# Kernel optimization log

Measured on AMD Instinct MI355X. Metric: run time of the kernel, lower is better.

## Reference

```python
import jax, jax.numpy as jnp
import numpy as np

EPS = 1e-5


def conv2d(x, w, b=None, stride=1, padding=0, dilation=1, groups=1):
    out = jax.lax.conv_general_dilated(
        x, w, (stride, stride), [(padding, padding), (padding, padding)],
        rhs_dilation=(dilation, dilation),
        dimension_numbers=('NCHW', 'OIHW', 'NCHW'),
        feature_group_count=groups)
    if b is not None:
        out = out + b[None, :, None, None]
    return out


def unfold3(x):
    # torch nn.Unfold(kernel=3, padding=1), kept as [b, c, 9, h, w]
    # (channel-major ordering c*9+k, k = row-major kernel index, matches torch)
    b, c, h, w = x.shape
    xp = jnp.pad(x, ((0, 0), (0, 0), (1, 1), (1, 1)))
    return jnp.stack([xp[:, :, i:i + h, j:j + w]
                      for i in range(3) for j in range(3)], axis=2)


def setup_inputs():
    B, C, O, H, W = 8, 64, 64, 128, 128
    key = jax.random.key(0)
    ks = jax.random.split(key, 16)
    s = 0.05
    rn = lambda k, shape: jax.random.normal(k, shape, jnp.float32) * s
    return {
        'x': jax.random.normal(ks[0], (B, C, H, W), jnp.float32),
        'cdcm_conv1_w': rn(ks[1], (C, C, 1, 1)),
        'cdcm_conv1_b': jnp.zeros((C,), jnp.float32),
        'cdcm_w5': rn(ks[2], (C, C, 3, 3)),
        'cdcm_w7': rn(ks[3], (C, C, 3, 3)),
        'cdcm_w9': rn(ks[4], (C, C, 3, 3)),
        'cdcm_w11': rn(ks[5], (C, C, 3, 3)),
        'dsc_dw_w': rn(ks[6], (C, 1, 3, 3)),
        'dsc_dw_b': jnp.zeros((C,), jnp.float32),
        'dsc_pw_w': rn(ks[7], (C, C, 1, 1)),
        'dsc_pw_b': jnp.zeros((C,), jnp.float32),
        'gw_w': rn(ks[8], (C, 9, 9)),
        'gw_b': jnp.zeros((C, 9), jnp.float32),
        'gw_bn_g': jnp.ones((C, 9), jnp.float32),
        'gw_bn_b': jnp.zeros((C, 9), jnp.float32),
        'gw_bn_m': jnp.zeros((C, 9), jnp.float32),
        'gw_bn_v': jnp.ones((C, 9), jnp.float32),
        'conv_w': rn(ks[9], (O, C, 3, 3)),
        'conv_b': jnp.zeros((O,), jnp.float32),
        'fr_w': rn(ks[10], (O, O, 1, 1)),
        'fr_b': jnp.zeros((O,), jnp.float32),
        'ens_w': rn(ks[11], (3, O, O, 3, 3)),
        'ens_b': jnp.zeros((3, O), jnp.float32),
        'bn_g': jnp.ones((O,), jnp.float32),
        'bn_b': jnp.zeros((O,), jnp.float32),
        'bn_m': jnp.zeros((O,), jnp.float32),
        'bn_v': jnp.ones((O,), jnp.float32),
    }


def reference(x, cdcm_conv1_w, cdcm_conv1_b, cdcm_w5, cdcm_w7, cdcm_w9, cdcm_w11,
              dsc_dw_w, dsc_dw_b, dsc_pw_w, dsc_pw_b,
              gw_w, gw_b, gw_bn_g, gw_bn_b, gw_bn_m, gw_bn_v,
              conv_w, conv_b, fr_w, fr_b, ens_w, ens_b,
              bn_g, bn_b, bn_m, bn_v):
    C = x.shape[1]
    # ---- CDCM: relu -> 1x1 conv -> 4 dilated 3x3 convs, each through the
    # SAME DepthwiseSeparableConv instance, then summed ----
    y = conv2d(jax.nn.relu(x), cdcm_conv1_w, cdcm_conv1_b)

    def dsc(z):
        z = conv2d(z, dsc_dw_w, dsc_dw_b, padding=1, groups=C)
        return conv2d(z, dsc_pw_w, dsc_pw_b)

    y = sum(dsc(conv2d(y, w, padding=d, dilation=d))
            for w, d in ((cdcm_w5, 5), (cdcm_w7, 7), (cdcm_w9, 9), (cdcm_w11, 11)))

    b, c, h, w = y.shape
    patches = unfold3(y)  # [b, c, 9, h, w]

    # ---- dynamic weight generation: grouped 1x1 conv (groups=c, 9->9 per
    # group) + inference BatchNorm over the c*9 channels + softmax over the 9
    # patch positions ----
    gw = jnp.einsum('coi,bcihw->bcohw', gw_w, patches) + gw_b[None, :, :, None, None]
    scale = (gw_bn_g / jnp.sqrt(gw_bn_v + EPS))[None, :, :, None, None]
    gw = (gw - gw_bn_m[None, :, :, None, None]) * scale + gw_bn_b[None, :, :, None, None]
    wsm = jax.nn.softmax(gw, axis=2)

    # ---- involution core: the rearrange to (3h,3w) + stride-3 3x3 conv is
    # exactly a contraction of (patches * weights) with the conv kernel over
    # the 9 kernel positions (row-major kernel index == patch index) ----
    prod = patches * wsm  # [b, c, 9, h, w]
    O = conv_w.shape[0]
    out = jnp.einsum('bckhw,ock->bohw', prod, conv_w.reshape(O, c, 9)) + conv_b[None, :, None, None]

    # ---- feature reuse: conv1x1(conv_out) + conv_out ----
    out = conv2d(out, fr_w, fr_b) + out

    # ---- ensemble: mean of 3 conv3x3 ----
    out = jnp.mean(jnp.stack([conv2d(out, ens_w[i], ens_b[i], padding=1)
                              for i in range(3)]), axis=0)

    # ---- final BN (inference) + ReLU ----
    out = (out - bn_m[None, :, None, None]) * (bn_g / jnp.sqrt(bn_v + EPS))[None, :, None, None] \
          + bn_b[None, :, None, None]
    return jax.nn.relu(out)
```

## Files before the change

### kernel.cpp

```cpp
#include <hip/hip_runtime.h>
#include <hip/hip_bf16.h>
#include <hip/hip_fp16.h>

#define EPSV 1e-5f
#define Bn 8
#define Cn 64
#define Hn 128
#define Wn 128
#define Pn (Hn*Wn)
#define PR 150
#define PE 130
#define YPAD_ELEMS (Bn*PR*PR*Cn)

typedef _Float16 v8h __attribute__((ext_vector_type(8)));
typedef float v16f __attribute__((ext_vector_type(16)));
typedef unsigned short ushort8v __attribute__((ext_vector_type(8)));
typedef unsigned short ushort4v __attribute__((ext_vector_type(4)));

__device__ __forceinline__ unsigned short f2h(float v) {
  _Float16 h = (_Float16)v;
  return *reinterpret_cast<const unsigned short*>(&h);
}
__device__ __forceinline__ float h2f(unsigned short u) {
  return (float)(*reinterpret_cast<const _Float16*>(&u));
}

__device__ __forceinline__ v8h exp8h(v8h x) {
  union { v8h v; __half2 h[4]; } u; u.v = x;
  #pragma unroll
  for (int i = 0; i < 4; i++) u.h[i] = h2exp(u.h[i]);
  return u.v;
}
__device__ __forceinline__ v8h rcp8h(v8h x) {
  union { v8h v; __half2 h[4]; } u; u.v = x;
  #pragma unroll
  for (int i = 0; i < 4; i++) u.h[i] = h2rcp(u.h[i]);
  return u.v;
}

__device__ __forceinline__ size_t clb(int b, int row, int kb, int col, int PD) {
  return ((((size_t)b * PD + row) * 4 + kb) * PD + col) * 16;
}

__device__ __forceinline__ void swz_bh(int& b, int& h) {
  int bid = blockIdx.x;
  int w = (bid & 7) * 128 + (bid >> 3);
  b = w >> 7; h = w & 127;
}

__global__ __launch_bounds__(256) void k_prep(
    const float* __restrict__ w1, const float* __restrict__ w5,
    const float* __restrict__ w7, const float* __restrict__ w9,
    const float* __restrict__ w11, const float* __restrict__ pww,
    const float* __restrict__ frw, const float* __restrict__ cw,
    const float* __restrict__ gww, const float* __restrict__ gwb,
    const float* __restrict__ gbg, const float* __restrict__ gbb,
    const float* __restrict__ gbm, const float* __restrict__ gbv,
    const float* __restrict__ ensw, const float* __restrict__ ensb,
    const float* __restrict__ bng, const float* __restrict__ bnb,
    const float* __restrict__ bnm, const float* __restrict__ bnv,
    unsigned short* __restrict__ apack, unsigned short* __restrict__ apinv,
    unsigned short* __restrict__ apens, unsigned short* __restrict__ appw1,
    unsigned short* __restrict__ appw, unsigned short* __restrict__ apfr,
    unsigned short* __restrict__ gwpk,
    unsigned short* __restrict__ apk, unsigned short* __restrict__ bpk,
    float* __restrict__ esc, float* __restrict__ ebi)
{
  int id = blockIdx.x * 256 + threadIdx.x;
  if (id < 147456) {
    int e = id & 7, l = (id >> 3) & 63, mh = (id >> 9) & 1,
        kb = (id >> 10) & 3, tap = id >> 12;
    int d = tap / 9, k9 = tap - 9 * d;
    int m = mh * 32 + (l & 31);
    int c = kb * 16 + (l >> 5) * 8 + e;
    const float* src = (d == 0) ? w5 : (d == 1) ? w7 : (d == 2) ? w9 : w11;
    apack[id] = f2h(src[(m * 64 + c) * 9 + k9]);
    return;
  }
  id -= 147456;
  if (id < 36864) {
    int e = id & 7, l = (id >> 3) & 63, mh = (id >> 9) & 1,
        kb = (id >> 10) & 3, tap = id >> 12;
    int m = mh * 32 + (l & 31);
    int c = kb * 16 + (l >> 5) * 8 + e;
    apinv[id] = f2h(cw[(m * 64 + c) * 9 + tap]);
    return;
  }
  id -= 36864;
  if (id < 36864) {
    int e = id & 7, l = (id >> 3) & 63, mh = (id >> 9) & 1,
        kb = (id >> 10) & 3, tap = id >> 12;
    int m = mh * 32 + (l & 31);
    int c = kb * 16 + (l >> 5) * 8 + e;
    float v = (ensw[((0 * 64 + m) * 64 + c) * 9 + tap] +
               ensw[((64 + m) * 64 + c) * 9 + tap] +
               ensw[((128 + m) * 64 + c) * 9 + tap]) * (1.f / 3.f);
    apens[id] = f2h(v);
    return;
  }
  id -= 36864;
  if (id < 4096) {
    int e = id & 7, l = (id >> 3) & 63, mh = (id >> 9) & 1, kb = (id >> 10) & 3;
    int m = mh * 32 + (l & 31);
    int c = kb * 16 + (l >> 5) * 8 + e;
    appw1[id] = f2h(w1[m * 64 + c]);
    return;
  }
  id -= 4096;
  if (id < 4096) {
    int e = id & 7, l = (id >> 3) & 63, mh = (id >> 9) & 1, kb = (id >> 10) & 3;
    int m = mh * 32 + (l & 31);
    int c = kb * 16 + (l >> 5) * 8 + e;
    appw[id] = f2h(pww[m * 64 + c]);
    return;
  }
  id -= 4096;
  if (id < 4096) {
    int e = id & 7, l = (id >> 3) & 63, mh = (id >> 9) & 1, kb = (id >> 10) & 3;
    int m = mh * 32 + (l & 31);
    int c = kb * 16 + (l >> 5) * 8 + e;
    apfr[id] = f2h(frw[m * 64 + c]);
    return;
  }
  id -= 4096;
  if (id < 5184) {
    int cblk = id / 648, r = id - cblk * 648;
    int tap = r >> 3, ch = r & 7;
    int c = cblk * 8 + ch;
    gwpk[id] = f2h(gww[c * 81 + tap]);
    return;
  }
  id -= 5184;
  if (id < 576) {
    int cblk = id / 72, r = id - cblk * 72;
    int o = r >> 3, ch = r & 7;
    int c = cblk * 8 + ch;
    float A = gbg[c * 9 + o] / sqrtf(gbv[c * 9 + o] + EPSV);
    apk[id] = f2h(A);
    return;
  }
  id -= 576;
  if (id < 576) {
    int cblk = id / 72, r = id - cblk * 72;
    int o = r >> 3, ch = r & 7;
    int c = cblk * 8 + ch;
    float A = gbg[c * 9 + o] / sqrtf(gbv[c * 9 + o] + EPSV);
    float B = (gwb[c * 9 + o] - gbm[c * 9 + o]) * A + gbb[c * 9 + o];
    bpk[id] = f2h(B);
    return;
  }
  id -= 576;
  if (id < 64) {
    float s = bng[id] / sqrtf(bnv[id] + EPSV);
    esc[id] = s;
    float bm = (ensb[id] + ensb[64 + id] + ensb[128 + id]) * (1.f / 3.f);
    ebi[id] = (bm - bnm[id]) * s + bnb[id];
  }
}

__global__ __launch_bounds__(256) void k_zb(unsigned short* __restrict__ buf,
                                            int PD, int pad)
{
  int per_b = 2 * pad * PD + 128 * 2 * pad;
  int id = blockIdx.x * 256 + threadIdx.x;
  int b = id / per_b;
  if (b >= Bn) return;
  int r = id - b * per_b;
  int tb = 2 * pad * PD;
  int row, col;
  if (r < tb) {
    int rr = r / PD; col = r - rr * PD;
    row = (rr < pad) ? rr : (rr + 128);
  } else {
    int r2 = r - tb;
    row = pad + r2 / (2 * pad);
    int cc = r2 - (r2 / (2 * pad)) * (2 * pad);
    col = (cc < pad) ? cc : (cc + 128);
  }
  ushort8v z = {0, 0, 0, 0, 0, 0, 0, 0};
  #pragma unroll
  for (int kb = 0; kb < 4; kb++) {
    unsigned short* p = buf + clb(b, row, kb, col, PD);
    *(ushort8v*)p = z;
    *(ushort8v*)(p + 8) = z;
  }
}

__global__ __launch_bounds__(256, 4) void k_pw1x(const float* __restrict__ x,
    const unsigned short* __restrict__ apw, const float* __restrict__ bias,
    unsigned short* __restrict__ ypad)
{
  int b, h; swz_bh(b, h);
  const int tid = threadIdx.x, wv = tid >> 6, l = tid & 63;
  const int ln31 = l & 31, g = l >> 5;
  const int px = wv * 32 + ln31;
  const float* xb = x + ((size_t)b * Cn) * Pn + h * Wn + px;
  v16f acc0, acc1;
  #pragma unroll
  for (int r = 0; r < 16; r++) { acc0[r] = 0.f; acc1[r] = 0.f; }
  const unsigned short* apl = apw + l * 8;
  #pragma unroll
  for (int kb = 0; kb < 4; kb++) {
    int c0 = kb * 16 + g * 8;
    v8h Bf;
    #pragma unroll
    for (int e = 0; e < 8; e++)
      Bf[e] = (_Float16)fmaxf(xb[(size_t)(c0 + e) * Pn], 0.f);
    v8h A0 = *(const v8h*)(apl + (kb * 2) * 512);
    v8h A1 = *(const v8h*)(apl + (kb * 2 + 1) * 512);
    acc0 = __builtin_amdgcn_mfma_f32_32x32x16_f16(A0, Bf, acc0, 0, 0, 0);
    acc1 = __builtin_amdgcn_mfma_f32_32x32x16_f16(A1, Bf, acc1, 0, 0, 0);
  }
  #pragma unroll
  for (int t = 0; t < 4; t++) {
    int c0 = 8 * t + 4 * g;
    int kb = c0 >> 4, sub = c0 & 15;
    ushort4v s0, s1;
    #pragma unroll
    for (int u = 0; u < 4; u++) {
      s0[u] = f2h(acc0[4 * t + u] + bias[c0 + u]);
      s1[u] = f2h(acc1[4 * t + u] + bias[c0 + u + 32]);
    }
    *(ushort4v*)(ypad + clb(b, h + 11, kb, px + 11, PR) + sub) = s0;
    *(ushort4v*)(ypad + clb(b, h + 11, kb + 2, px + 11, PR) + sub) = s1;
  }
}

__global__ __launch_bounds__(256) void k_cdcm_mfma(
    const unsigned short* __restrict__ ypad,
    const unsigned short* __restrict__ apack,
    unsigned short* __restrict__ spad)
{
  __shared__ __align__(16) unsigned short Abuf[36864];
  const int bid = blockIdx.x;
  const int b = bid & 7, h0 = (bid >> 3) * 2;
  const int tid = threadIdx.x, wv = tid >> 6, l = tid & 63;
  const int ln31 = l & 31, g = l >> 5;

  v16f a00, a01, a10, a11;
  #pragma unroll
  for (int r = 0; r < 16; r++) { a00[r] = 0.f; a01[r] = 0.f; a10[r] = 0.f; a11[r] = 0.f; }

  const unsigned short* abl = Abuf + l * 8;

  for (int d = 0; d < 4; d++) {
    __syncthreads();
    {
      const ushort8v* src = (const ushort8v*)(apack + d * 36864);
      ushort8v* dst = (ushort8v*)Abuf;
      #pragma unroll
      for (int it = 0; it < 18; it++)
        dst[tid + it * 256] = src[tid + it * 256];
    }
    __syncthreads();

    const int dil = 5 + 2 * d;
    #pragma unroll
    for (int ky = 0; ky < 3; ky++) {
      const int r0 = h0 + 11 + (ky - 1) * dil;
      #pragma unroll
      for (int kx = 0; kx < 3; kx++) {
        const int col = wv * 32 + ln31 + (kx - 1) * dil + 11;
        const int t9 = ky * 3 + kx;
        const unsigned short* ap = abl + t9 * 4096;
        #pragma unroll
        for (int kb = 0; kb < 4; kb++) {
          v8h B0 = *(const v8h*)(ypad + clb(b, r0, kb, col, PR) + g * 8);
          v8h B1 = *(const v8h*)(ypad + clb(b, r0 + 1, kb, col, PR) + g * 8);
          v8h A0 = *(const v8h*)(ap + kb * 1024);
          v8h A1 = *(const v8h*)(ap + kb * 1024 + 512);
          a00 = __builtin_amdgcn_mfma_f32_32x32x16_f16(A0, B0, a00, 0, 0, 0);
          a01 = __builtin_amdgcn_mfma_f32_32x32x16_f16(A1, B0, a01, 0, 0, 0);
          a10 = __builtin_amdgcn_mfma_f32_32x32x16_f16(A0, B1, a10, 0, 0, 0);
          a11 = __builtin_amdgcn_mfma_f32_32x32x16_f16(A1, B1, a11, 0, 0, 0);
        }
      }
    }
  }
  const int px = wv * 32 + ln31;
  #pragma unroll
  for (int t = 0; t < 4; t++) {
    int c0 = 8 * t + 4 * g;
    int kb = c0 >> 4, sub = c0 & 15;
    ushort4v s0, s1, s2, s3;
    #pragma unroll
    for (int u = 0; u < 4; u++) {
      s0[u] = f2h(a00[4 * t + u]);
      s1[u] = f2h(a01[4 * t + u]);
      s2[u] = f2h(a10[4 * t + u]);
      s3[u] = f2h(a11[4 * t + u]);
    }
    *(ushort4v*)(spad + clb(b, h0 + 1, kb, px + 1, PE) + sub) = s0;
    *(ushort4v*)(spad + clb(b, h0 + 1, kb + 2, px + 1, PE) + sub) = s1;
    *(ushort4v*)(spad + clb(b, h0 + 2, kb, px + 1, PE) + sub) = s2;
    *(ushort4v*)(spad + clb(b, h0 + 2, kb + 2, px + 1, PE) + sub) = s3;
  }
}

__global__ __launch_bounds__(256, 4) void k_dwpw_mfma(
    const unsigned short* __restrict__ spad,
    const float* __restrict__ dww, const float* __restrict__ dwb,
    const unsigned short* __restrict__ appw, const float* __restrict__ pwb,
    unsigned short* __restrict__ y2pad)
{
  __shared__ float wdw[576];
  __shared__ float bdw[64];
  const int tid = threadIdx.x;
  for (int t = tid; t < 576; t += 256) wdw[t] = dww[t];
  if (tid < 64) bdw[tid] = dwb[tid];
  __syncthreads();

  int b, h; swz_bh(b, h);
  const int wv = tid >> 6, l = tid & 63;
  const int ln31 = l & 31, g = l >> 5;
  const int w = wv * 32 + ln31;

  v16f acc0, acc1;
  #pragma unroll
  for (int r = 0; r < 16; r++) { acc0[r] = 0.f; acc1[r] = 0.f; }
  const unsigned short* apl = appw + l * 8;

  #pragma unroll
  for (int kb = 0; kb < 4; kb++) {
    const int c0 = kb * 16 + g * 8;
    v8h t[9];
    #pragma unroll
    for (int k = 0; k < 9; k++) {
      const int dy = k / 3 - 1, dx = k % 3 - 1;
      t[k] = *(const v8h*)(spad + clb(b, h + 1 + dy, kb, w + 1 + dx, PE) + g * 8);
    }
    v8h dvh;
    #pragma unroll
    for (int e = 0; e < 8; e++) {
      const int c = c0 + e;
      float a = 4.f * bdw[c];
      #pragma unroll
      for (int k = 0; k < 9; k++) a += wdw[c * 9 + k] * (float)t[k][e];
      dvh[e] = (_Float16)a;
    }
    v8h A0 = *(const v8h*)(apl + (kb * 2) * 512);
    v8h A1 = *(const v8h*)(apl + (kb * 2 + 1) * 512);
    acc0 = __builtin_amdgcn_mfma_f32_32x32x16_f16(A0, dvh, acc0, 0, 0, 0);
    acc1 = __builtin_amdgcn_mfma_f32_32x32x16_f16(A1, dvh, acc1, 0, 0, 0);
  }
  #pragma unroll
  for (int t = 0; t < 4; t++) {
    int c0 = 8 * t + 4 * g;
    int kb = c0 >> 4, sub = c0 & 15;
    ushort4v s0, s1;
    #pragma unroll
    for (int u = 0; u < 4; u++) {
      s0[u] = f2h(acc0[4 * t + u] + 4.f * pwb[c0 + u]);
      s1[u] = f2h(acc1[4 * t + u] + 4.f * pwb[c0 + u + 32]);
    }
    *(ushort4v*)(y2pad + clb(b, h + 1, kb, w + 1, PE) + sub) = s0;
    *(ushort4v*)(y2pad + clb(b, h + 1, kb + 2, w + 1, PE) + sub) = s1;
  }
}

__global__ __launch_bounds__(256, 3) void k_invol_mfma(
    const unsigned short* __restrict__ y2pad,
    const unsigned short* __restrict__ gwpk,
    const unsigned short* __restrict__ apk,
    const unsigned short* __restrict__ bpk,
    const unsigned short* __restrict__ apinv,
    const float* __restrict__ cbias,
    unsigned short* __restrict__ ipad)
{
  __shared__ __align__(16) unsigned short gws[5184];
  __shared__ __align__(16) unsigned short As[576];
  __shared__ __align__(16) unsigned short Bs[576];
  const int tid = threadIdx.x;
  for (int t = tid; t < 648; t += 256)
    ((ushort8v*)gws)[t] = ((const ushort8v*)gwpk)[t];
  if (tid < 72) {
    ((ushort8v*)As)[tid] = ((const ushort8v*)apk)[tid];
    ((ushort8v*)Bs)[tid] = ((const ushort8v*)bpk)[tid];
  }
  __syncthreads();

  int b, h; swz_bh(b, h);
  const int wv = tid >> 6, l = tid & 63;
  const int p32 = l & 31, g = l >> 5;
  const int w = wv * 32 + p32;

  v16f acc0, acc1;
  #pragma unroll
  for (int r = 0; r < 16; r++) { acc0[r] = 0.f; acc1[r] = 0.f; }

  for (int cb4 = 0; cb4 < 4; cb4++) {
    const int cblk = cb4 * 2 + g;
    const unsigned short* gwp = gws + cblk * 648;
    const unsigned short* Ap = As + cblk * 72;
    const unsigned short* Bp = Bs + cblk * 72;

    v8h pt[9];
    #pragma unroll
    for (int k = 0; k < 9; k++) {
      const int dy = k / 3 - 1, dx = k % 3 - 1;
      pt[k] = *(const v8h*)(y2pad + clb(b, h + 1 + dy, cb4, w + 1 + dx, PE) + g * 8);
    }
    v8h s[9];
    #pragma unroll
    for (int o = 0; o < 9; o++) {
      v8h a = (*(const v8h*)(gwp + o * 72)) * pt[0];
      #pragma unroll
      for (int i = 1; i < 9; i++)
        a += (*(const v8h*)(gwp + o * 72 + i * 8)) * pt[i];
      s[o] = a * (*(const v8h*)(Ap + o * 8)) + (*(const v8h*)(Bp + o * 8));
    }
    v8h esum = {0, 0, 0, 0, 0, 0, 0, 0};
    #pragma unroll
    for (int o = 0; o < 9; o++) { s[o] = exp8h(s[o]); esum += s[o]; }
    v8h inv = rcp8h(esum);
    #pragma unroll
    for (int k = 0; k < 9; k++) pt[k] = pt[k] * s[k] * inv;

    const unsigned short* ap = apinv + l * 8;
    #pragma unroll
    for (int k = 0; k < 9; k++) {
      const unsigned short* a2 = ap + ((k * 4 + cb4) * 2) * 512;
      v8h A0 = *(const v8h*)(a2);
      v8h A1 = *(const v8h*)(a2 + 512);
      acc0 = __builtin_amdgcn_mfma_f32_32x32x16_f16(A0, pt[k], acc0, 0, 0, 0);
      acc1 = __builtin_amdgcn_mfma_f32_32x32x16_f16(A1, pt[k], acc1, 0, 0, 0);
    }
  }
  #pragma unroll
  for (int t = 0; t < 4; t++) {
    int c0 = 8 * t + 4 * g;
    int kb = c0 >> 4, sub = c0 & 15;
    ushort4v s0, s1;
    #pragma unroll
    for (int u = 0; u < 4; u++) {
      s0[u] = f2h(acc0[4 * t + u] + cbias[c0 + u]);
      s1[u] = f2h(acc1[4 * t + u] + cbias[c0 + u + 32]);
    }
    *(ushort4v*)(ipad + clb(b, h, kb, w, 128) + sub) = s0;
    *(ushort4v*)(ipad + clb(b, h, kb + 2, w, 128) + sub) = s1;
  }
}

__global__ __launch_bounds__(256, 4) void k_fr_mfma(
    const unsigned short* __restrict__ ipad,
    const unsigned short* __restrict__ apfr,
    const float* __restrict__ bias,
    unsigned short* __restrict__ opad)
{
  int b, h; swz_bh(b, h);
  const int tid = threadIdx.x, wv = tid >> 6, l = tid & 63;
  const int ln31 = l & 31, g = l >> 5;
  const int px = wv * 32 + ln31;
  v16f acc0, acc1;
  #pragma unroll
  for (int r = 0; r < 16; r++) { acc0[r] = 0.f; acc1[r] = 0.f; }
  const unsigned short* apl = apfr + l * 8;
  #pragma unroll
  for (int kb = 0; kb < 4; kb++) {
    v8h Bf = *(const v8h*)(ipad + clb(b, h, kb, px, 128) + g * 8);
    v8h A0 = *(const v8h*)(apl + (kb * 2) * 512);
    v8h A1 = *(const v8h*)(apl + (kb * 2 + 1) * 512);
    acc0 = __builtin_amdgcn_mfma_f32_32x32x16_f16(A0, Bf, acc0, 0, 0, 0);
    acc1 = __builtin_amdgcn_mfma_f32_32x32x16_f16(A1, Bf, acc1, 0, 0, 0);
  }
  #pragma unroll
  for (int t = 0; t < 4; t++) {
    int c0 = 8 * t + 4 * g;
    int kb = c0 >> 4, sub = c0 & 15;
    ushort4v r0 = *(const ushort4v*)(ipad + clb(b, h, kb, px, 128) + sub);
    ushort4v r1 = *(const ushort4v*)(ipad + clb(b, h, kb + 2, px, 128) + sub);
    ushort4v s0, s1;
    #pragma unroll
    for (int u = 0; u < 4; u++) {
      s0[u] = f2h(acc0[4 * t + u] + bias[c0 + u] + h2f(r0[u]));
      s1[u] = f2h(acc1[4 * t + u] + bias[c0 + u + 32] + h2f(r1[u]));
    }
    *(ushort4v*)(opad + clb(b, h + 1, kb, px + 1, PE) + sub) = s0;
    *(ushort4v*)(opad + clb(b, h + 1, kb + 2, px + 1, PE) + sub) = s1;
  }
}

__global__ __launch_bounds__(256) void k_ens_mfma(
    const unsigned short* __restrict__ opad,
    const unsigned short* __restrict__ apens,
    const float* __restrict__ esc, const float* __restrict__ ebi,
    float* __restrict__ out)
{
  __shared__ __align__(16) unsigned short Abuf[36864];
  const int tid = threadIdx.x;
  {
    const ushort8v* src = (const ushort8v*)apens;
    ushort8v* dst = (ushort8v*)Abuf;
    #pragma unroll
    for (int it = 0; it < 18; it++)
      dst[tid + it * 256] = src[tid + it * 256];
  }
  __syncthreads();

  const int bid = blockIdx.x;
  const int b = bid & 7, h0 = (bid >> 3) * 2;
  const int wv = tid >> 6, l = tid & 63;
  const int ln31 = l & 31, g = l >> 5;

  v16f a00, a01, a10, a11;
  #pragma unroll
  for (int r = 0; r < 16; r++) { a00[r] = 0.f; a01[r] = 0.f; a10[r] = 0.f; a11[r] = 0.f; }

  const unsigned short* abl = Abuf + l * 8;

  #pragma unroll
  for (int ky = 0; ky < 3; ky++) {
    #pragma unroll
    for (int kx = 0; kx < 3; kx++) {
      const int tap = ky * 3 + kx;
      const int r0 = h0 + ky;
      const int col = wv * 32 + ln31 + kx;
      const unsigned short* ap = abl + tap * 4096;
      #pragma unroll
      for (int kb = 0; kb < 4; kb++) {
        v8h B0 = *(const v8h*)(opad + clb(b, r0, kb, col, PE) + g * 8);
        v8h B1 = *(const v8h*)(opad + clb(b, r0 + 1, kb, col, PE) + g * 8);
        v8h A0 = *(const v8h*)(ap + kb * 1024);
        v8h A1 = *(const v8h*)(ap + kb * 1024 + 512);
        a00 = __builtin_amdgcn_mfma_f32_32x32x16_f16(A0, B0, a00, 0, 0, 0);
        a01 = __builtin_amdgcn_mfma_f32_32x32x16_f16(A1, B0, a01, 0, 0, 0);
        a10 = __builtin_amdgcn_mfma_f32_32x32x16_f16(A0, B1, a10, 0, 0, 0);
        a11 = __builtin_amdgcn_mfma_f32_32x32x16_f16(A1, B1, a11, 0, 0, 0);
      }
    }
  }
  float* sp0 = out + ((size_t)b * Cn) * Pn + h0 * Wn + wv * 32 + ln31;
  float* sp1 = sp0 + Wn;
  #pragma unroll
  for (int r = 0; r < 16; r++) {
    int o0 = (r & 3) + 8 * (r >> 2) + 4 * g;
    float e0 = esc[o0], e1 = esc[o0 + 32];
    float i0 = ebi[o0], i1 = ebi[o0 + 32];
    sp0[(size_t)o0 * Pn] = fmaxf(a00[r] * e0 + i0, 0.f);
    sp0[(size_t)(o0 + 32) * Pn] = fmaxf(a01[r] * e1 + i1, 0.f);
    sp1[(size_t)o0 * Pn] = fmaxf(a10[r] * e0 + i0, 0.f);
    sp1[(size_t)(o0 + 32) * Pn] = fmaxf(a11[r] * e1 + i1, 0.f);
  }
}

extern "C" void kernel_launch(void* const* d_in, const int* in_sizes, int n_in,
                              void* d_out, int out_size, void* d_ws, size_t ws_size,
                              hipStream_t stream)
{
  const float* x    = (const float*)d_in[0];
  const float* w1   = (const float*)d_in[1];
  const float* b1   = (const float*)d_in[2];
  const float* w5   = (const float*)d_in[3];
  const float* w7   = (const float*)d_in[4];
  const float* w9   = (const float*)d_in[5];
  const float* w11  = (const float*)d_in[6];
  const float* dww  = (const float*)d_in[7];
  const float* dwb  = (const float*)d_in[8];
  const float* pww  = (const float*)d_in[9];
  const float* pwb  = (const float*)d_in[10];
  const float* gww  = (const float*)d_in[11];
  const float* gwb  = (const float*)d_in[12];
  const float* gbg  = (const float*)d_in[13];
  const float* gbb  = (const float*)d_in[14];
  const float* gbm  = (const float*)d_in[15];
  const float* gbv  = (const float*)d_in[16];
  const float* cw   = (const float*)d_in[17];
  const float* cb   = (const float*)d_in[18];
  const float* frw  = (const float*)d_in[19];
  const float* frb  = (const float*)d_in[20];
  const float* ensw = (const float*)d_in[21];
  const float* ensb = (const float*)d_in[22];
  const float* bng  = (const float*)d_in[23];
  const float* bnb  = (const float*)d_in[24];
  const float* bnm  = (const float*)d_in[25];
  const float* bnv  = (const float*)d_in[26];

  unsigned short* wsu   = (unsigned short*)d_ws;
  unsigned short* ypad  = wsu;
  unsigned short* y2pad = wsu;
  unsigned short* opad  = wsu;
  unsigned short* apack = wsu + YPAD_ELEMS;
  unsigned short* apinv = apack + 147456;
  unsigned short* apens = apinv + 36864;
  unsigned short* appw1 = apens + 36864;
  unsigned short* appw  = appw1 + 4096;
  unsigned short* apfr  = appw + 4096;
  unsigned short* gwpk  = apfr + 4096;
  unsigned short* apk   = gwpk + 5184;
  unsigned short* bpk   = apk + 576;
  float* esc = (float*)(bpk + 576);
  float* ebi = esc + 64;

  unsigned short* spad = (unsigned short*)d_out;
  unsigned short* ipad = (unsigned short*)d_out;
  float* D = (float*)d_out;

  k_prep<<<937, 256, 0, stream>>>(w1, w5, w7, w9, w11, pww, frw, cw,
                                  gww, gwb, gbg, gbb, gbm, gbv, ensw, ensb,
                                  bng, bnb, bnm, bnv,
                                  apack, apinv, apens, appw1, appw, apfr,
                                  gwpk, apk, bpk, esc, ebi);
  k_zb<<<192, 256, 0, stream>>>(ypad, PR, 11);
  k_zb<<<17, 256, 0, stream>>>(spad, PE, 1);

  k_pw1x<<<1024, 256, 0, stream>>>(x, appw1, b1, ypad);
  k_cdcm_mfma<<<512, 256, 0, stream>>>(ypad, apack, spad);
  k_zb<<<17, 256, 0, stream>>>(y2pad, PE, 1);
  k_dwpw_mfma<<<1024, 256, 0, stream>>>(spad, dww, dwb, appw, pwb, y2pad);
  k_invol_mfma<<<1024, 256, 0, stream>>>(y2pad, gwpk, apk, bpk, apinv, cb, ipad);
  k_fr_mfma<<<1024, 256, 0, stream>>>(ipad, apfr, frb, opad);
  k_ens_mfma<<<512, 256, 0, stream>>>(opad, apens, esc, ebi, D);
}
```

Measured before the change: 164.7 us.

## Halve CDCM LDS tile, one row per block, fold border zeroing into other kernels

The dilated CDCM kernel now computes one output row per block instead of two. The weight slice staged in LDS is cut in half by splitting the channel blocks into two passes, and the kernel gets launch_bounds(256,4) for higher occupancy. The grid doubles to 1024 blocks, and the weight pack layout is reordered to match. The separate zero-border kernels are removed: ypad/spad border zeroing moves into k_prep and y2pad zeroing into k_dwpw, which drops three launches. In exchange, weights are reloaded per row and there are more syncthreads, with no reuse of A across two rows.

```diff
diff --git a/kernel.cpp b/kernel.cpp
--- a/kernel.cpp
+++ b/kernel.cpp
@@ -64,17 +64,20 @@
     unsigned short* __restrict__ appw, unsigned short* __restrict__ apfr,
     unsigned short* __restrict__ gwpk,
     unsigned short* __restrict__ apk, unsigned short* __restrict__ bpk,
-    float* __restrict__ esc, float* __restrict__ ebi)
+    float* __restrict__ esc, float* __restrict__ ebi,
+    unsigned short* __restrict__ ypad, unsigned short* __restrict__ spad)
 {
   int id = blockIdx.x * 256 + threadIdx.x;
   if (id < 147456) {
     int e = id & 7, l = (id >> 3) & 63, mh = (id >> 9) & 1,
-        kb = (id >> 10) & 3, tap = id >> 12;
-    int d = tap / 9, k9 = tap - 9 * d;
+        kbl = (id >> 10) & 1;
+    int r2 = id >> 11;
+    int t9 = r2 % 9; int dk = r2 / 9;
+    int kbp = dk & 1, d = dk >> 1;
     int m = mh * 32 + (l & 31);
-    int c = kb * 16 + (l >> 5) * 8 + e;
+    int c = (kbp * 2 + kbl) * 16 + (l >> 5) * 8 + e;
     const float* src = (d == 0) ? w5 : (d == 1) ? w7 : (d == 2) ? w9 : w11;
-    apack[id] = f2h(src[(m * 64 + c) * 9 + k9]);
+    apack[id] = f2h(src[(m * 64 + c) * 9 + t9]);
     return;
   }
   id -= 147456;
@@ -155,34 +158,52 @@
     esc[id] = s;
     float bm = (ensb[id] + ensb[64 + id] + ensb[128 + id]) * (1.f / 3.f);
     ebi[id] = (bm - bnm[id]) * s + bnb[id];
-  }
-}
-
-__global__ __launch_bounds__(256) void k_zb(unsigned short* __restrict__ buf,
-                                            int PD, int pad)
-{
-  int per_b = 2 * pad * PD + 128 * 2 * pad;
-  int id = blockIdx.x * 256 + threadIdx.x;
-  int b = id / per_b;
-  if (b >= Bn) return;
-  int r = id - b * per_b;
-  int tb = 2 * pad * PD;
-  int row, col;
-  if (r < tb) {
-    int rr = r / PD; col = r - rr * PD;
-    row = (rr < pad) ? rr : (rr + 128);
-  } else {
-    int r2 = r - tb;
-    row = pad + r2 / (2 * pad);
-    int cc = r2 - (r2 / (2 * pad)) * (2 * pad);
-    col = (cc < pad) ? cc : (cc + 128);
-  }
+    return;
+  }
+  id -= 64;
   ushort8v z = {0, 0, 0, 0, 0, 0, 0, 0};
-  #pragma unroll
-  for (int kb = 0; kb < 4; kb++) {
-    unsigned short* p = buf + clb(b, row, kb, col, PD);
-    *(ushort8v*)p = z;
-    *(ushort8v*)(p + 8) = z;
+  const int perY = 22 * PR + 128 * 22;
+  if (id < perY * Bn) {
+    int b = id / perY; int r = id - b * perY;
+    int tb = 22 * PR;
+    int row, col;
+    if (r < tb) {
+      int rr = r / PR; col = r - rr * PR;
+      row = (rr < 11) ? rr : (rr + 128);
+    } else {
+      int r2 = r - tb;
+      row = 11 + r2 / 22;
+      int cc = r2 % 22;
+      col = (cc < 11) ? cc : (cc + 128);
+    }
+    #pragma unroll
+    for (int kb = 0; kb < 4; kb++) {
+      unsigned short* p = ypad + clb(b, row, kb, col, PR);
+      *(ushort8v*)p = z;
+      *(ushort8v*)(p + 8) = z;
+    }
+    return;
+  }
+  id -= perY * Bn;
+  const int perS = 2 * PE + 256;
+  if (id < perS * Bn) {
+    int b = id / perS; int r = id - b * perS;
+    int tb = 2 * PE;
+    int row, col;
+    if (r < tb) {
+      int rr = r / PE; col = r - rr * PE;
+      row = (rr < 1) ? 0 : 129;
+    } else {
+      int r2 = r - tb;
+      row = 1 + r2 / 2;
+      col = (r2 & 1) ? 129 : 0;
+    }
+    #pragma unroll
+    for (int kb = 0; kb < 4; kb++) {
+      unsigned short* p = spad + clb(b, row, kb, col, PE);
+      *(ushort8v*)p = z;
+      *(ushort8v*)(p + 8) = z;
+    }
   }
 }
 
@@ -226,53 +247,51 @@
   }
 }
 
-__global__ __launch_bounds__(256) void k_cdcm_mfma(
+__global__ __launch_bounds__(256, 4) void k_cdcm_mfma(
     const unsigned short* __restrict__ ypad,
     const unsigned short* __restrict__ apack,
     unsigned short* __restrict__ spad)
 {
-  __shared__ __align__(16) unsigned short Abuf[36864];
-  const int bid = blockIdx.x;
-  const int b = bid & 7, h0 = (bid >> 3) * 2;
+  __shared__ __align__(16) unsigned short Abuf[18432];
+  int b, h; swz_bh(b, h);
   const int tid = threadIdx.x, wv = tid >> 6, l = tid & 63;
   const int ln31 = l & 31, g = l >> 5;
 
-  v16f a00, a01, a10, a11;
-  #pragma unroll
-  for (int r = 0; r < 16; r++) { a00[r] = 0.f; a01[r] = 0.f; a10[r] = 0.f; a11[r] = 0.f; }
+  v16f acc0, acc1;
+  #pragma unroll
+  for (int r = 0; r < 16; r++) { acc0[r] = 0.f; acc1[r] = 0.f; }
 
   const unsigned short* abl = Abuf + l * 8;
 
   for (int d = 0; d < 4; d++) {
-    __syncthreads();
-    {
-      const ushort8v* src = (const ushort8v*)(apack + d * 36864);
-      ushort8v* dst = (ushort8v*)Abuf;
+    const int dil = 5 + 2 * d;
+    for (int kbp = 0; kbp < 2; kbp++) {
+      __syncthreads();
+      {
+        const ushort8v* src = (const ushort8v*)(apack + (d * 2 + kbp) * 18432);
+        ushort8v* dst = (ushort8v*)Abuf;
+        #pragma unroll
+        for (int it = 0; it < 9; it++)
+          dst[tid + it * 256] = src[tid + it * 256];
+      }
+      __syncthreads();
       #pragma unroll
-      for (int it = 0; it < 18; it++)
-        dst[tid + it * 256] = src[tid + it * 256];
-    }
-    __syncthreads();
-
-    const int dil = 5 + 2 * d;
-    #pragma unroll
-    for (int ky = 0; ky < 3; ky++) {
-      const int r0 = h0 + 11 + (ky - 1) * dil;
-      #pragma unroll
-      for (int kx = 0; kx < 3; kx++) {
-        const int col = wv * 32 + ln31 + (kx - 1) * dil + 11;
-        const int t9 = ky * 3 + kx;
-        const unsigned short* ap = abl + t9 * 4096;
+      for (int ky = 0; ky < 3; ky++) {
+        const int row = h + 11 + (ky - 1) * dil;
         #pragma unroll
-        for (int kb = 0; kb < 4; kb++) {
-          v8h B0 = *(const v8h*)(ypad + clb(b, r0, kb, col, PR) + g * 8);
-          v8h B1 = *(const v8h*)(ypad + clb(b, r0 + 1, kb, col, PR) + g * 8);
-          v8h A0 = *(const v8h*)(ap + kb * 1024);
-          v8h A1 = *(const v8h*)(ap + kb * 1024 + 512);
-          a00 = __builtin_amdgcn_mfma_f32_32x32x16_f16(A0, B0, a00, 0, 0, 0);
-          a01 = __builtin_amdgcn_mfma_f32_32x32x16_f16(A1, B0, a01, 0, 0, 0);
-          a10 = __builtin_amdgcn_mfma_f32_32x32x16_f16(A0, B1, a10, 0, 0, 0);
-          a11 = __builtin_amdgcn_mfma_f32_32x32x16_f16(A1, B1, a11, 0, 0, 0);
+        for (int kx = 0; kx < 3; kx++) {
+          const int col = wv * 32 + ln31 + (kx - 1) * dil + 11;
+          const int t9 = ky * 3 + kx;
+          #pragma unroll
+          for (int kbl = 0; kbl < 2; kbl++) {
+            const int kb = kbp * 2 + kbl;
+            v8h Bf = *(const v8h*)(ypad + clb(b, row, kb, col, PR) + g * 8);
+            const unsigned short* ap = abl + (t9 * 2 + kbl) * 1024;
+            v8h A0 = *(const v8h*)(ap);
+            v8h A1 = *(const v8h*)(ap + 512);
+            acc0 = __builtin_amdgcn_mfma_f32_32x32x16_f16(A0, Bf, acc0, 0, 0, 0);
+            acc1 = __builtin_amdgcn_mfma_f32_32x32x16_f16(A1, Bf, acc1, 0, 0, 0);
+          }
         }
       }
     }
@@ -282,18 +301,14 @@
   for (int t = 0; t < 4; t++) {
     int c0 = 8 * t + 4 * g;
     int kb = c0 >> 4, sub = c0 & 15;
-    ushort4v s0, s1, s2, s3;
+    ushort4v s0, s1;
     #pragma unroll
     for (int u = 0; u < 4; u++) {
-      s0[u] = f2h(a00[4 * t + u]);
-      s1[u] = f2h(a01[4 * t + u]);
-      s2[u] = f2h(a10[4 * t + u]);
-      s3[u] = f2h(a11[4 * t + u]);
-    }
-    *(ushort4v*)(spad + clb(b, h0 + 1, kb, px + 1, PE) + sub) = s0;
-    *(ushort4v*)(spad + clb(b, h0 + 1, kb + 2, px + 1, PE) + sub) = s1;
-    *(ushort4v*)(spad + clb(b, h0 + 2, kb, px + 1, PE) + sub) = s2;
-    *(ushort4v*)(spad + clb(b, h0 + 2, kb + 2, px + 1, PE) + sub) = s3;
+      s0[u] = f2h(acc0[4 * t + u]);
+      s1[u] = f2h(acc1[4 * t + u]);
+    }
+    *(ushort4v*)(spad + clb(b, h + 1, kb, px + 1, PE) + sub) = s0;
+    *(ushort4v*)(spad + clb(b, h + 1, kb + 2, px + 1, PE) + sub) = s1;
   }
 }
 
@@ -311,6 +326,30 @@
   __syncthreads();
 
   int b, h; swz_bh(b, h);
+
+  ushort8v z = {0, 0, 0, 0, 0, 0, 0, 0};
+  if (h == 0) {
+    for (int px = tid; px < 260; px += 256) {
+      int row = (px < 130) ? 0 : 129;
+      int col = (px < 130) ? px : px - 130;
+      #pragma unroll
+      for (int kb = 0; kb < 4; kb++) {
+        unsigned short* p = y2pad + clb(b, row, kb, col, PE);
+        *(ushort8v*)p = z;
+        *(ushort8v*)(p + 8) = z;
+      }
+    }
+  } else if (h == 1) {
+    int row = 1 + (tid & 127);
+    int col = (tid >> 7) ? 129 : 0;
+    #pragma unroll
+    for (int kb = 0; kb < 4; kb++) {
+      unsigned short* p = y2pad + clb(b, row, kb, col, PE);
+      *(ushort8v*)p = z;
+      *(ushort8v*)(p + 8) = z;
+    }
+  }
+
   const int wv = tid >> 6, l = tid & 63;
   const int ln31 = l & 31, g = l >> 5;
   const int w = wv * 32 + ln31;
@@ -595,17 +634,15 @@
   unsigned short* ipad = (unsigned short*)d_out;
   float* D = (float*)d_out;
 
-  k_prep<<<937, 256, 0, stream>>>(w1, w5, w7, w9, w11, pww, frw, cw,
-                                  gww, gwb, gbg, gbb, gbm, gbv, ensw, ensb,
-                                  bng, bnb, bnm, bnv,
-                                  apack, apinv, apens, appw1, appw, apfr,
-                                  gwpk, apk, bpk, esc, ebi);
-  k_zb<<<192, 256, 0, stream>>>(ypad, PR, 11);
-  k_zb<<<17, 256, 0, stream>>>(spad, PE, 1);
+  k_prep<<<1145, 256, 0, stream>>>(w1, w5, w7, w9, w11, pww, frw, cw,
+                                   gww, gwb, gbg, gbb, gbm, gbv, ensw, ensb,
+                                   bng, bnb, bnm, bnv,
+                                   apack, apinv, apens, appw1, appw, apfr,
+                                   gwpk, apk, bpk, esc, ebi,
+                                   ypad, spad);
 
   k_pw1x<<<1024, 256, 0, stream>>>(x, appw1, b1, ypad);
-  k_cdcm_mfma<<<512, 256, 0, stream>>>(ypad, apack, spad);
-  k_zb<<<17, 256, 0, stream>>>(y2pad, PE, 1);
+  k_cdcm_mfma<<<1024, 256, 0, stream>>>(ypad, apack, spad);
   k_dwpw_mfma<<<1024, 256, 0, stream>>>(spad, dww, dwb, appw, pwb, y2pad);
   k_invol_mfma<<<1024, 256, 0, stream>>>(y2pad, gwpk, apk, bpk, apinv, cb, ipad);
   k_fr_mfma<<<1024, 256, 0, stream>>>(ipad, apfr, frb, opad);
```

After: 160.8 us. 1.02x faster.
